# Optimization experiments

Hardware: AMD Instinct MI355X
Metric: run time of the kernel (lower is better)

Reference implementation:

```python
import jax, jax.numpy as jnp
import numpy as np

D_MODEL = 1024
D_HEAD = 64
B, S = 4, 4096


def setup_inputs() -> dict:
    key = jax.random.key(0)
    ks = jax.random.split(key, 7)
    inv = 1.0 / np.sqrt(D_MODEL)
    return {
        "x": jax.random.normal(ks[0], (B, S, D_MODEL), dtype=jnp.float32),
        "W_q": jax.random.normal(ks[1], (D_MODEL, D_HEAD), dtype=jnp.float32) * inv,
        "b_q": jax.random.normal(ks[2], (D_HEAD,), dtype=jnp.float32) * 0.02,
        "W_k": jax.random.normal(ks[3], (D_MODEL, D_HEAD), dtype=jnp.float32) * inv,
        "b_k": jax.random.normal(ks[4], (D_HEAD,), dtype=jnp.float32) * 0.02,
        "W_v": jax.random.normal(ks[5], (D_MODEL, D_HEAD), dtype=jnp.float32) * inv,
        "b_v": jax.random.normal(ks[6], (D_HEAD,), dtype=jnp.float32) * 0.02,
    }


def reference(x, W_q, b_q, W_k, b_k, W_v, b_v):
    # Projections: [B, S, d_head]
    Q = jnp.einsum("bsd,dh->bsh", x, W_q) + b_q
    K = jnp.einsum("bsd,dh->bsh", x, W_k) + b_k
    V = jnp.einsum("bsd,dh->bsh", x, W_v) + b_v
    scale = 1.0 / jnp.sqrt(jnp.asarray(Q.shape[-1], dtype=Q.dtype))
    scores = jnp.einsum("bqh,bkh->bqk", Q, K) * scale  # [B, S, S]
    seq_len = x.shape[1]
    causal = jnp.tril(jnp.ones((seq_len, seq_len), dtype=bool))
    scores = jnp.where(causal, scores, jnp.asarray(-jnp.inf, dtype=scores.dtype))
    A = jax.nn.softmax(scores, axis=-1)
    return jnp.einsum("bqk,bkh->bqh", A, V)  # [B, S, d_head]
```

## Files before the change

kernel.cpp:

```cpp
#include <hip/hip_runtime.h>

typedef __attribute__((ext_vector_type(4))) float f32x4;
typedef __attribute__((ext_vector_type(8))) short short8;
typedef unsigned short ushort_t;

constexpr int DM = 1024, DH = 64, S = 4096, B = 4;
constexpr float QSCALE = 0.125f * 1.44269504088896340736f;
constexpr int SPLIT = 4;

constexpr size_t WBT_OFF = 0;
constexpr size_t QB_OFF  = 393216;
constexpr size_t KB_OFF  = QB_OFF + 2097152;
constexpr size_t VT_OFF  = KB_OFF + 2097152;
constexpr size_t ML_OFF  = VT_OFF + 2097152;
constexpr size_t PO_OFF  = ML_OFF + 524288;

__device__ __forceinline__ ushort_t f2bf(float f) {
    unsigned u = __float_as_uint(f);
    u += 0x7FFFu + ((u >> 16) & 1u);
    return (ushort_t)(u >> 16);
}

__device__ __forceinline__ void gl_lds16(const void* g, void* l) {
    __builtin_amdgcn_global_load_lds(
        (const __attribute__((address_space(1))) unsigned int*)g,
        (__attribute__((address_space(3))) unsigned int*)l, 16, 0, 0);
}

__global__ __launch_bounds__(256) void prep_w_kernel(
    const float* __restrict__ Wq, const float* __restrict__ Wk,
    const float* __restrict__ Wv, ushort_t* __restrict__ wbt)
{
    const int n = blockIdx.x;
    const int p = n >> 6, d = n & 63;
    const float* W = (p == 0) ? Wq : (p == 1) ? Wk : Wv;
    const int k0 = threadIdx.x * 4;
    ushort4 pack;
    pack.x = f2bf(W[(k0 + 0) * DH + d]);
    pack.y = f2bf(W[(k0 + 1) * DH + d]);
    pack.z = f2bf(W[(k0 + 2) * DH + d]);
    pack.w = f2bf(W[(k0 + 3) * DH + d]);
    *reinterpret_cast<ushort4*>(wbt + (size_t)n * DM + k0) = pack;
}

__global__ __launch_bounds__(512, 4) void qkv_mfma_kernel(
    const float* __restrict__ x, const ushort_t* __restrict__ wbt,
    const float* __restrict__ bq, const float* __restrict__ bk,
    const float* __restrict__ bv,
    ushort_t* __restrict__ qb, ushort_t* __restrict__ kb, ushort_t* __restrict__ vt)
{
    __shared__ uint4 AsU[2][256];
    __shared__ uint4 BsU[2][768];

    const int tid = threadIdx.x;
    const int wid = tid >> 6, lane = tid & 63;
    const int q16 = lane & 15, lg = lane >> 4;
    const int sub = wid & 1, np = wid >> 1;
    const int r0 = blockIdx.x * 32;
    const char* xB = (const char*)x;
    const char* wB = (const char*)wbt;

    auto task = [&](int tk, int buf, int kk) {
        if (tk < 4) {
            gl_lds16(xB + (size_t)(r0 + tk * 8 + (lane >> 3)) * 4096 + kk * 4
                        + (((lane & 7) ^ (lane >> 3)) << 4),
                     (char*)&AsU[buf][0] + tk * 1024 + lane * 16);
        } else {
            const int sg = tk - 4;
            gl_lds16(wB + (size_t)(sg * 16 + (lane >> 2)) * 2048 + kk * 2
                        + ((((lane & 3) ^ ((lane >> 2) & 3))) << 4),
                     (char*)&BsU[buf][0] + sg * 1024 + lane * 16);
        }
    };

    f32x4 acc[3];
#pragma unroll
    for (int j = 0; j < 3; ++j) acc[j] = {0.f, 0.f, 0.f, 0.f};

    task(2 * wid, 0, 0);
    task(2 * wid + 1, 0, 0);
    __syncthreads();

    const int row = sub * 16 + q16;
    for (int s = 0; s < 32; ++s) {
        const int buf = s & 1;
        if (s + 1 < 32) {
            task(2 * wid, buf ^ 1, (s + 1) * 32);
            task(2 * wid + 1, buf ^ 1, (s + 1) * 32);
        }
        const char* AsC = (const char*)&AsU[buf][0];
        const char* BsC = (const char*)&BsU[buf][0];
        const f32x4 a0 = *(const f32x4*)(AsC + row * 128 + (((2 * lg) ^ (row & 7)) << 4));
        const f32x4 a1 = *(const f32x4*)(AsC + row * 128 + (((2 * lg + 1) ^ (row & 7)) << 4));
        short8 Af;
        Af[0] = (short)f2bf(a0[0]); Af[1] = (short)f2bf(a0[1]);
        Af[2] = (short)f2bf(a0[2]); Af[3] = (short)f2bf(a0[3]);
        Af[4] = (short)f2bf(a1[0]); Af[5] = (short)f2bf(a1[1]);
        Af[6] = (short)f2bf(a1[2]); Af[7] = (short)f2bf(a1[3]);
        __builtin_amdgcn_s_setprio(1);
#pragma unroll
        for (int j = 0; j < 3; ++j) {
            const int nt = np * 3 + j;
            const short8 Bf = *(const short8*)(
                BsC + (nt * 16 + q16) * 64 + ((lg ^ (q16 & 3)) << 4));
            acc[j] = __builtin_amdgcn_mfma_f32_16x16x32_bf16(Af, Bf, acc[j], 0, 0, 0);
        }
        __builtin_amdgcn_s_setprio(0);
        __syncthreads();
    }

#pragma unroll
    for (int j = 0; j < 3; ++j) {
        const int nt = np * 3 + j;
        const int p = nt >> 2, d = ((nt & 3) << 4) + q16;
        const float* bp = (p == 0) ? bq : (p == 1) ? bk : bv;
        const float bb = bp[d];
#pragma unroll
        for (int r = 0; r < 4; ++r) {
            const int m = r0 + sub * 16 + (lg << 2) + r;
            const float v = acc[j][r] + bb;
            if (p == 0) {
                qb[(size_t)m * 64 + d] = f2bf(v * QSCALE);
            } else if (p == 1) {
                kb[(size_t)m * 64 + d] = f2bf(v);
            } else {
                const int bb_ = m >> 12, sx = m & 4095;
                vt[(size_t)bb_ * 262144 + (size_t)d * 4096 + sx] = f2bf(v);
            }
        }
    }
}

__global__ __launch_bounds__(256, 4) void attn_mfma_kernel(
    const ushort_t* __restrict__ qb, const ushort_t* __restrict__ kb,
    const ushort_t* __restrict__ vt, ushort_t* __restrict__ po,
    float* __restrict__ ml)
{
    __shared__ uint4 LsU[2][1024];
    __shared__ uint2 PsU[4][256];

    const int tid = threadIdx.x;
    const int wid = tid >> 6, lane = tid & 63;
    const int q16 = lane & 15, lg = lane >> 4;
    const int z = blockIdx.y;

    const int linear = blockIdx.x;
    const int xcd = linear & 7, idx = linear >> 3;
    const int b = xcd >> 1;
    const int qt = 63 - (idx * 2 + (xcd & 1));

    const int qrow = qt * 64 + wid * 16 + q16;
    const ushort_t* Qb = qb + (size_t)b * S * 64;
    const char* KbB = (const char*)(kb + (size_t)b * S * 64);
    const char* VtB = (const char*)(vt + (size_t)b * 64 * S);

    const short8 qf0 = *(const short8*)(Qb + (size_t)qrow * 64 + lg * 8);
    const short8 qf1 = *(const short8*)(Qb + (size_t)qrow * 64 + 32 + lg * 8);

    f32x4 o[4];
#pragma unroll
    for (int nt = 0; nt < 4; ++nt) o[nt] = {0.f, 0.f, 0.f, 0.f};
    float m = -1e30f, l = 0.f;

    char* PsC = (char*)&PsU[wid][0];
    const int ntiles = qt + 1;

    auto stage = [&](int t, int buf) {
        const int kv0 = t * 64;
#pragma unroll
        for (int i = 0; i < 4; ++i) {
            const int slot = i * 256 + tid;
            char* dst = (char*)&LsU[buf][0] + slot * 16;
            if (slot < 512) {
                const int row = slot >> 3, ch = slot & 7;
                gl_lds16(KbB + (size_t)(kv0 + row) * 128 + ((ch ^ (row & 7)) << 4), dst);
            } else {
                const int d = (slot - 512) >> 3, ch = slot & 7;
                gl_lds16(VtB + (size_t)d * (S * 2) + kv0 * 2 + ((ch ^ (d & 7)) << 4), dst);
            }
        }
    };

    int buf = 0;
    if (z < ntiles) stage(z, 0);
    __syncthreads();

    for (int t = z; t < ntiles; t += SPLIT) {
        if (t + SPLIT < ntiles) stage(t + SPLIT, buf ^ 1);
        const char* KsC = (const char*)&LsU[buf][0];
        const char* VsC = KsC + 8192;
        const int kv0 = t * 64;

        f32x4 st[4];
#pragma unroll
        for (int mt = 0; mt < 4; ++mt) st[mt] = {0.f, 0.f, 0.f, 0.f};
#pragma unroll
        for (int ks = 0; ks < 2; ++ks) {
            short8 kf[4];
#pragma unroll
            for (int mt = 0; mt < 4; ++mt)
                kf[mt] = *(const short8*)(
                    KsC + (mt * 16 + q16) * 128 + (((lg + 4 * ks) ^ (q16 & 7)) << 4));
            __builtin_amdgcn_s_setprio(1);
#pragma unroll
            for (int mt = 0; mt < 4; ++mt)
                st[mt] = __builtin_amdgcn_mfma_f32_16x16x32_bf16(
                    kf[mt], (ks ? qf1 : qf0), st[mt], 0, 0, 0);
            __builtin_amdgcn_s_setprio(0);
        }

        if (t == ntiles - 1) {
#pragma unroll
            for (int mt = 0; mt < 4; ++mt)
#pragma unroll
                for (int r = 0; r < 4; ++r)
                    if (kv0 + mt * 16 + (lg << 2) + r > qrow) st[mt][r] = -1e30f;
        }

        float tm = -1e30f;
#pragma unroll
        for (int mt = 0; mt < 4; ++mt)
#pragma unroll
            for (int r = 0; r < 4; ++r) tm = fmaxf(tm, st[mt][r]);
        tm = fmaxf(tm, __shfl_xor(tm, 16));
        tm = fmaxf(tm, __shfl_xor(tm, 32));
        const float mn = fmaxf(m, tm);
        const float corr = exp2f(m - mn);
        float ps = 0.f;
#pragma unroll
        for (int mt = 0; mt < 4; ++mt)
#pragma unroll
            for (int r = 0; r < 4; ++r) {
                const float pv = exp2f(st[mt][r] - mn);
                st[mt][r] = pv;
                ps += pv;
            }
        ps += __shfl_xor(ps, 16);
        ps += __shfl_xor(ps, 32);
        l = l * corr + ps;
        m = mn;

        float corr_row[4];
#pragma unroll
        for (int r = 0; r < 4; ++r) corr_row[r] = __shfl(corr, (lg << 2) | r);
#pragma unroll
        for (int nt = 0; nt < 4; ++nt)
#pragma unroll
            for (int r = 0; r < 4; ++r) o[nt][r] *= corr_row[r];

#pragma unroll
        for (int mt = 0; mt < 4; ++mt) {
            uint2 w;
            w.x = (unsigned)f2bf(st[mt][0]) | ((unsigned)f2bf(st[mt][1]) << 16);
            w.y = (unsigned)f2bf(st[mt][2]) | ((unsigned)f2bf(st[mt][3]) << 16);
            const int ch = (2 * mt + (lg >> 1)) ^ (q16 & 7);
            *reinterpret_cast<uint2*>(PsC + q16 * 128 + ch * 16 + (lg & 1) * 8) = w;
        }
        const short8 pa0 = *reinterpret_cast<const short8*>(
            PsC + q16 * 128 + ((lg ^ (q16 & 7)) << 4));
        const short8 pa1 = *reinterpret_cast<const short8*>(
            PsC + q16 * 128 + (((lg + 4) ^ (q16 & 7)) << 4));

        __builtin_amdgcn_s_setprio(1);
#pragma unroll
        for (int ks = 0; ks < 2; ++ks) {
            const short8 pa = ks ? pa1 : pa0;
#pragma unroll
            for (int nt = 0; nt < 4; ++nt) {
                const short8 vf = *(const short8*)(
                    VsC + (nt * 16 + q16) * 128 + (((lg + 4 * ks) ^ (q16 & 7)) << 4));
                o[nt] = __builtin_amdgcn_mfma_f32_16x16x32_bf16(pa, vf, o[nt], 0, 0, 0);
            }
        }
        __builtin_amdgcn_s_setprio(0);

        __syncthreads();
        buf ^= 1;
    }

    const int rowbase = qt * 64 + wid * 16;
    const size_t zb = (size_t)z * B * S + (size_t)b * S;
#pragma unroll
    for (int nt = 0; nt < 4; ++nt)
#pragma unroll
        for (int r = 0; r < 4; ++r)
            po[(zb + rowbase + (lg << 2) + r) * 64 + nt * 16 + q16] = f2bf(o[nt][r]);
    if (lg == 0) {
        ml[(zb + rowbase + q16) * 2 + 0] = m;
        ml[(zb + rowbase + q16) * 2 + 1] = l;
    }
}

__global__ __launch_bounds__(256) void merge_kernel(
    const ushort_t* __restrict__ po, const float* __restrict__ ml,
    float* __restrict__ out)
{
    const int idx = blockIdx.x * 256 + threadIdx.x;
    const int row = idx >> 3, c8 = idx & 7;

    float mv[SPLIT], lv[SPLIT];
#pragma unroll
    for (int zz = 0; zz < SPLIT; ++zz) {
        const float2 t = *(const float2*)(ml + ((size_t)zz * B * S + row) * 2);
        mv[zz] = t.x; lv[zz] = t.y;
    }
    const float mm = fmaxf(fmaxf(mv[0], mv[1]), fmaxf(mv[2], mv[3]));
    float L = 0.f, cz[SPLIT];
#pragma unroll
    for (int zz = 0; zz < SPLIT; ++zz) { cz[zz] = exp2f(mv[zz] - mm); L += lv[zz] * cz[zz]; }
    const float inv = 1.0f / L;

    float acc[8];
#pragma unroll
    for (int e = 0; e < 8; ++e) acc[e] = 0.f;
#pragma unroll
    for (int zz = 0; zz < SPLIT; ++zz) {
        const uint4 pk = *(const uint4*)(po + ((size_t)zz * B * S + row) * 64 + c8 * 8);
        const unsigned w[4] = {pk.x, pk.y, pk.z, pk.w};
#pragma unroll
        for (int i = 0; i < 4; ++i) {
            acc[2 * i + 0] += cz[zz] * __uint_as_float((w[i] & 0xFFFFu) << 16);
            acc[2 * i + 1] += cz[zz] * __uint_as_float((w[i] >> 16) << 16);
        }
    }
    float4 o0 = make_float4(acc[0] * inv, acc[1] * inv, acc[2] * inv, acc[3] * inv);
    float4 o1 = make_float4(acc[4] * inv, acc[5] * inv, acc[6] * inv, acc[7] * inv);
    *(float4*)(out + (size_t)row * 64 + c8 * 8 + 0) = o0;
    *(float4*)(out + (size_t)row * 64 + c8 * 8 + 4) = o1;
}

extern "C" void kernel_launch(void* const* d_in, const int* in_sizes, int n_in,
                              void* d_out, int out_size, void* d_ws, size_t ws_size,
                              hipStream_t stream) {
    const float* x  = (const float*)d_in[0];
    const float* Wq = (const float*)d_in[1];
    const float* bq = (const float*)d_in[2];
    const float* Wk = (const float*)d_in[3];
    const float* bk = (const float*)d_in[4];
    const float* Wv = (const float*)d_in[5];
    const float* bv = (const float*)d_in[6];
    float* out = (float*)d_out;

    char* ws = (char*)d_ws;
    ushort_t* wbt = (ushort_t*)(ws + WBT_OFF);
    ushort_t* qbp = (ushort_t*)(ws + QB_OFF);
    ushort_t* kbp = (ushort_t*)(ws + KB_OFF);
    ushort_t* vtp = (ushort_t*)(ws + VT_OFF);
    float*    mlp = (float*)(ws + ML_OFF);
    ushort_t* pop = (ushort_t*)(ws + PO_OFF);

    hipLaunchKernelGGL(prep_w_kernel, dim3(192), dim3(256), 0, stream, Wq, Wk, Wv, wbt);
    hipLaunchKernelGGL(qkv_mfma_kernel, dim3(512), dim3(512), 0, stream,
                       x, wbt, bq, bk, bv, qbp, kbp, vtp);
    hipLaunchKernelGGL(attn_mfma_kernel, dim3(256, SPLIT), dim3(256), 0, stream,
                       qbp, kbp, vtp, pop, mlp);
    hipLaunchKernelGGL(merge_kernel, dim3(512), dim3(256), 0, stream, pop, mlp, out);
}
```

Baseline: 79.53 us.

## Double KV tile to 128, skip rescale when max unchanged, use packed bf16 convert

The attention kernel now processes 128 keys per tile instead of 64, doubling the K/V staging buffers and the P scratch in LDS, and widening the swizzle to 16 chunks. This halves the number of barrier and softmax-bookkeeping iterations per query tile. It also adds a wave-uniform fast path that skips the output rescale when no row's max increases, and swaps the manual bf16 rounding for the hardware packed convert instruction. The cost is about twice the LDS per block, which may limit occupancy under the 4-blocks-per-CU launch bound, plus more registers for the scores. The causal tail tile now covers 128 keys, so more fully masked work is done on the diagonal.

```diff
diff --git a/kernel.cpp b/kernel.cpp
--- a/kernel.cpp
+++ b/kernel.cpp
@@ -19,6 +19,12 @@
     unsigned u = __float_as_uint(f);
     u += 0x7FFFu + ((u >> 16) & 1u);
     return (ushort_t)(u >> 16);
+}
+
+__device__ __forceinline__ unsigned cvt_pk_bf16(float lo, float hi) {
+    unsigned r;
+    asm volatile("v_cvt_pk_bf16_f32 %0, %1, %2" : "=v"(r) : "v"(lo), "v"(hi));
+    return r;
 }
 
 __device__ __forceinline__ void gl_lds16(const void* g, void* l) {
@@ -136,8 +142,8 @@
     const ushort_t* __restrict__ vt, ushort_t* __restrict__ po,
     float* __restrict__ ml)
 {
-    __shared__ uint4 LsU[2][1024];
-    __shared__ uint2 PsU[4][256];
+    __shared__ uint4 LsU[2][2048];
+    __shared__ uint4 PsU[4][256];
 
     const int tid = threadIdx.x;
     const int wid = tid >> 6, lane = tid & 63;
@@ -163,20 +169,21 @@
     float m = -1e30f, l = 0.f;
 
     char* PsC = (char*)&PsU[wid][0];
-    const int ntiles = qt + 1;
+    const int ntiles = (qt >> 1) + 1;
 
     auto stage = [&](int t, int buf) {
-        const int kv0 = t * 64;
-#pragma unroll
-        for (int i = 0; i < 4; ++i) {
+        const int kv0 = t * 128;
+#pragma unroll
+        for (int i = 0; i < 8; ++i) {
             const int slot = i * 256 + tid;
             char* dst = (char*)&LsU[buf][0] + slot * 16;
-            if (slot < 512) {
+            if (slot < 1024) {
                 const int row = slot >> 3, ch = slot & 7;
                 gl_lds16(KbB + (size_t)(kv0 + row) * 128 + ((ch ^ (row & 7)) << 4), dst);
             } else {
-                const int d = (slot - 512) >> 3, ch = slot & 7;
-                gl_lds16(VtB + (size_t)d * (S * 2) + kv0 * 2 + ((ch ^ (d & 7)) << 4), dst);
+                const int s2 = slot - 1024;
+                const int d = s2 >> 4, ch = s2 & 15;
+                gl_lds16(VtB + (size_t)d * (S * 2) + kv0 * 2 + ((ch ^ (d & 15)) << 4), dst);
             }
         }
     };
@@ -188,30 +195,35 @@
     for (int t = z; t < ntiles; t += SPLIT) {
         if (t + SPLIT < ntiles) stage(t + SPLIT, buf ^ 1);
         const char* KsC = (const char*)&LsU[buf][0];
-        const char* VsC = KsC + 8192;
-        const int kv0 = t * 64;
-
-        f32x4 st[4];
-#pragma unroll
-        for (int mt = 0; mt < 4; ++mt) st[mt] = {0.f, 0.f, 0.f, 0.f};
+        const char* VsC = KsC + 16384;
+        const int kv0 = t * 128;
+
+        f32x4 st[8];
+#pragma unroll
+        for (int mt = 0; mt < 8; ++mt) st[mt] = {0.f, 0.f, 0.f, 0.f};
 #pragma unroll
         for (int ks = 0; ks < 2; ++ks) {
-            short8 kf[4];
-#pragma unroll
-            for (int mt = 0; mt < 4; ++mt)
-                kf[mt] = *(const short8*)(
-                    KsC + (mt * 16 + q16) * 128 + (((lg + 4 * ks) ^ (q16 & 7)) << 4));
-            __builtin_amdgcn_s_setprio(1);
-#pragma unroll
-            for (int mt = 0; mt < 4; ++mt)
-                st[mt] = __builtin_amdgcn_mfma_f32_16x16x32_bf16(
-                    kf[mt], (ks ? qf1 : qf0), st[mt], 0, 0, 0);
-            __builtin_amdgcn_s_setprio(0);
+#pragma unroll
+            for (int mg = 0; mg < 2; ++mg) {
+                short8 kf[4];
+#pragma unroll
+                for (int j = 0; j < 4; ++j) {
+                    const int mt = mg * 4 + j;
+                    kf[j] = *(const short8*)(
+                        KsC + (mt * 16 + q16) * 128 + (((lg + 4 * ks) ^ (q16 & 7)) << 4));
+                }
+                __builtin_amdgcn_s_setprio(1);
+#pragma unroll
+                for (int j = 0; j < 4; ++j)
+                    st[mg * 4 + j] = __builtin_amdgcn_mfma_f32_16x16x32_bf16(
+                        kf[j], (ks ? qf1 : qf0), st[mg * 4 + j], 0, 0, 0);
+                __builtin_amdgcn_s_setprio(0);
+            }
         }
 
         if (t == ntiles - 1) {
 #pragma unroll
-            for (int mt = 0; mt < 4; ++mt)
+            for (int mt = 0; mt < 8; ++mt)
 #pragma unroll
                 for (int r = 0; r < 4; ++r)
                     if (kv0 + mt * 16 + (lg << 2) + r > qrow) st[mt][r] = -1e30f;
@@ -219,56 +231,68 @@
 
         float tm = -1e30f;
 #pragma unroll
-        for (int mt = 0; mt < 4; ++mt)
+        for (int mt = 0; mt < 8; ++mt)
 #pragma unroll
             for (int r = 0; r < 4; ++r) tm = fmaxf(tm, st[mt][r]);
         tm = fmaxf(tm, __shfl_xor(tm, 16));
         tm = fmaxf(tm, __shfl_xor(tm, 32));
-        const float mn = fmaxf(m, tm);
-        const float corr = exp2f(m - mn);
-        float ps = 0.f;
-#pragma unroll
-        for (int mt = 0; mt < 4; ++mt)
-#pragma unroll
-            for (int r = 0; r < 4; ++r) {
-                const float pv = exp2f(st[mt][r] - mn);
-                st[mt][r] = pv;
-                ps += pv;
-            }
-        ps += __shfl_xor(ps, 16);
-        ps += __shfl_xor(ps, 32);
-        l = l * corr + ps;
-        m = mn;
-
-        float corr_row[4];
-#pragma unroll
-        for (int r = 0; r < 4; ++r) corr_row[r] = __shfl(corr, (lg << 2) | r);
-#pragma unroll
-        for (int nt = 0; nt < 4; ++nt)
-#pragma unroll
-            for (int r = 0; r < 4; ++r) o[nt][r] *= corr_row[r];
-
-#pragma unroll
-        for (int mt = 0; mt < 4; ++mt) {
+
+        if (__all(tm <= m)) {
+            float ps = 0.f;
+#pragma unroll
+            for (int mt = 0; mt < 8; ++mt)
+#pragma unroll
+                for (int r = 0; r < 4; ++r) {
+                    const float pv = exp2f(st[mt][r] - m);
+                    st[mt][r] = pv;
+                    ps += pv;
+                }
+            ps += __shfl_xor(ps, 16);
+            ps += __shfl_xor(ps, 32);
+            l += ps;
+        } else {
+            const float mn = fmaxf(m, tm);
+            const float corr = exp2f(m - mn);
+            float ps = 0.f;
+#pragma unroll
+            for (int mt = 0; mt < 8; ++mt)
+#pragma unroll
+                for (int r = 0; r < 4; ++r) {
+                    const float pv = exp2f(st[mt][r] - mn);
+                    st[mt][r] = pv;
+                    ps += pv;
+                }
+            ps += __shfl_xor(ps, 16);
+            ps += __shfl_xor(ps, 32);
+            l = l * corr + ps;
+            m = mn;
+            float corr_row[4];
+#pragma unroll
+            for (int r = 0; r < 4; ++r) corr_row[r] = __shfl(corr, (lg << 2) | r);
+#pragma unroll
+            for (int nt = 0; nt < 4; ++nt)
+#pragma unroll
+                for (int r = 0; r < 4; ++r) o[nt][r] *= corr_row[r];
+        }
+
+#pragma unroll
+        for (int mt = 0; mt < 8; ++mt) {
             uint2 w;
-            w.x = (unsigned)f2bf(st[mt][0]) | ((unsigned)f2bf(st[mt][1]) << 16);
-            w.y = (unsigned)f2bf(st[mt][2]) | ((unsigned)f2bf(st[mt][3]) << 16);
-            const int ch = (2 * mt + (lg >> 1)) ^ (q16 & 7);
-            *reinterpret_cast<uint2*>(PsC + q16 * 128 + ch * 16 + (lg & 1) * 8) = w;
-        }
-        const short8 pa0 = *reinterpret_cast<const short8*>(
-            PsC + q16 * 128 + ((lg ^ (q16 & 7)) << 4));
-        const short8 pa1 = *reinterpret_cast<const short8*>(
-            PsC + q16 * 128 + (((lg + 4) ^ (q16 & 7)) << 4));
+            w.x = cvt_pk_bf16(st[mt][0], st[mt][1]);
+            w.y = cvt_pk_bf16(st[mt][2], st[mt][3]);
+            const int ch = (2 * mt + (lg >> 1)) ^ q16;
+            *reinterpret_cast<uint2*>(PsC + q16 * 256 + ch * 16 + (lg & 1) * 8) = w;
+        }
 
         __builtin_amdgcn_s_setprio(1);
 #pragma unroll
-        for (int ks = 0; ks < 2; ++ks) {
-            const short8 pa = ks ? pa1 : pa0;
+        for (int ks = 0; ks < 4; ++ks) {
+            const short8 pa = *reinterpret_cast<const short8*>(
+                PsC + q16 * 256 + (((4 * ks + lg) ^ q16) << 4));
 #pragma unroll
             for (int nt = 0; nt < 4; ++nt) {
                 const short8 vf = *(const short8*)(
-                    VsC + (nt * 16 + q16) * 128 + (((lg + 4 * ks) ^ (q16 & 7)) << 4));
+                    VsC + (nt * 16 + q16) * 256 + (((ks * 4 + lg) ^ q16) << 4));
                 o[nt] = __builtin_amdgcn_mfma_f32_16x16x32_bf16(pa, vf, o[nt], 0, 0, 0);
             }
         }
```

Result: faster. 72.78 us, median of 2 (-8.5%).
